# Kernel tuning notes

Measured on AMD Instinct MI355X. Metric: run time of the kernel, lower is better.

The kernel has to match this reference:

```python
import jax, jax.numpy as jnp
import numpy as np


def gru_last(x, lens, Wg, bg, Wc, bc):
    """TF GRUCell scan over time, masked by lens; returns final hidden state.
    x: [N, T, D], lens: [N] int, Wg: [D+H, 2H], Wc: [D+H, H]. Returns [N, H]."""
    N, T, _ = x.shape
    H = bc.shape[0]
    xT = jnp.swapaxes(x, 0, 1)  # [T, N, D]

    def step(h, inp):
        xt, t = inp
        ru = jax.nn.sigmoid(jnp.concatenate([xt, h], axis=-1) @ Wg + bg)
        r, u = jnp.split(ru, 2, axis=-1)
        c = jnp.tanh(jnp.concatenate([xt, r * h], axis=-1) @ Wc + bc)
        hn = u * h + (1.0 - u) * c
        hn = jnp.where((t < lens)[:, None], hn, h)
        return hn, None

    h0 = jnp.zeros((N, H), x.dtype)
    hT, _ = jax.lax.scan(step, h0, (xT, jnp.arange(T)))
    return hT


def reverse_by_len(x, lens):
    """tf.reverse_sequence: reverse first lens[i] steps of each row. x: [N,T,D]."""
    T = x.shape[1]
    i = jnp.arange(T)[None, :]
    idx = jnp.where(i < lens[:, None], lens[:, None] - 1 - i, i)
    return jnp.take_along_axis(x, idx[:, :, None], axis=1)


def setup_inputs() -> dict:
    key = jax.random.key(0)
    ks = jax.random.split(key, 16)
    B, S, W = 64, 32, 64
    V, D, H, O = 50000, 128, 256, 5
    s = 0.05
    inp = {
        'X': jax.random.randint(ks[0], (B, S, W), 0, V, dtype=jnp.int32),
        'L': jnp.maximum(1, jax.random.randint(ks[1], (B, S), 0, W, dtype=jnp.int32)),
        'L2': jnp.maximum(1, jax.random.randint(ks[2], (B,), 0, S, dtype=jnp.int32)),
        'emb': jax.random.normal(ks[3], (V, D), jnp.float32) * s,
        'sWg_f': jax.random.normal(ks[4], (2 * D, 2 * D), jnp.float32) * s,
        'sbg_f': jnp.ones((2 * D,), jnp.float32),
        'sWc_f': jax.random.normal(ks[5], (2 * D, D), jnp.float32) * s,
        'sbc_f': jnp.zeros((D,), jnp.float32),
        'sWg_b': jax.random.normal(ks[6], (2 * D, 2 * D), jnp.float32) * s,
        'sbg_b': jnp.ones((2 * D,), jnp.float32),
        'sWc_b': jax.random.normal(ks[7], (2 * D, D), jnp.float32) * s,
        'sbc_b': jnp.zeros((D,), jnp.float32),
        'dWg_f': jax.random.normal(ks[8], (2 * D + H, 2 * H), jnp.float32) * s,
        'dbg_f': jnp.ones((2 * H,), jnp.float32),
        'dWc_f': jax.random.normal(ks[9], (2 * D + H, H), jnp.float32) * s,
        'dbc_f': jnp.zeros((H,), jnp.float32),
        'dWg_b': jax.random.normal(ks[10], (2 * D + H, 2 * H), jnp.float32) * s,
        'dbg_b': jnp.ones((2 * H,), jnp.float32),
        'dWc_b': jax.random.normal(ks[11], (2 * D + H, H), jnp.float32) * s,
        'dbc_b': jnp.zeros((H,), jnp.float32),
        'W1': jax.random.normal(ks[12], (2 * H, H), jnp.float32) * s,
        'b1': jnp.zeros((H,), jnp.float32),
        'W2': jax.random.normal(ks[13], (H, O), jnp.float32) * s,
        'b2': jnp.zeros((O,), jnp.float32),
    }
    return inp


def reference(X, L, L2, emb,
              sWg_f, sbg_f, sWc_f, sbc_f, sWg_b, sbg_b, sWc_b, sbc_b,
              dWg_f, dbg_f, dWc_f, dbc_f, dWg_b, dbg_b, dWc_b, dbc_b,
              W1, b1, W2, b2):
    B, S, W = X.shape
    D = emb.shape[1]
    # word embeddings: [B, S, W, D] -> flatten sentences to rows
    words = emb[X].reshape(B * S, W, D)
    ls = L.reshape(B * S)
    # sentence-level bi-GRU, gather final valid states
    fw = gru_last(words, ls, sWg_f, sbg_f, sWc_f, sbc_f)
    bw = gru_last(reverse_by_len(words, ls), ls, sWg_b, sbg_b, sWc_b, sbc_b)
    sent = jnp.concatenate([fw, bw], axis=-1).reshape(B, S, 2 * D)
    # document-level bi-GRU over sentence vectors
    fw_d = gru_last(sent, L2, dWg_f, dbg_f, dWc_f, dbc_f)
    bw_d = gru_last(reverse_by_len(sent, L2), L2, dWg_b, dbg_b, dWc_b, dbc_b)
    doc = jnp.concatenate([fw_d, bw_d], axis=-1)  # [B, 2H]
    # MLP head
    hidden = jax.nn.relu(doc @ W1 + b1)
    logits = hidden @ W2 + b2
    return logits
```

## Files before the change

kernel.cpp:

```cpp
#include <hip/hip_runtime.h>
#include <cstdint>
#include <cstddef>


typedef __attribute__((ext_vector_type(8))) short bf16x8;
typedef __attribute__((ext_vector_type(8))) _Float16 f16x8;
typedef __attribute__((ext_vector_type(4))) float f32x4;

__device__ __forceinline__ void split_bf16(float f, short& hi, short& lo) {
  unsigned u = __float_as_uint(f);
  unsigned rb = (u + 0x7FFFu + ((u >> 16) & 1u)) & 0xFFFF0000u;
  hi = (short)(rb >> 16);
  float r = f - __uint_as_float(rb);
  unsigned ur = __float_as_uint(r);
  lo = (short)((ur + 0x7FFFu + ((ur >> 16) & 1u)) >> 16);
}

__device__ __forceinline__ void split_f16(float f, short& hi, short& lo) {
  _Float16 h = (_Float16)f;
  hi = __builtin_bit_cast(short, h);
  _Float16 l = (_Float16)(f - (float)h);
  lo = __builtin_bit_cast(short, l);
}

__device__ __forceinline__ float sigm(float x) { return 1.f / (1.f + __expf(-x)); }
__device__ __forceinline__ float tanh_fast(float x) {
  float e = __expf(2.f * x);
  return 1.f - 2.f / (e + 1.f);
}

__global__ void bt_prep(const float* __restrict__ sWg_f, const float* __restrict__ sWc_f,
                        const float* __restrict__ sWg_b, const float* __restrict__ sWc_b,
                        short* __restrict__ BtHi, short* __restrict__ BtLo) {
  int i = blockIdx.x * 256 + threadIdx.x;
  if (i >= 768 * 128) return;
  int n = i >> 7, k = i & 127;
  float f;
  if (n < 256) f = sWg_f[k * 256 + n];
  else if (n < 384) f = sWc_f[k * 128 + (n - 256)];
  else if (n < 640) f = sWg_b[k * 256 + (n - 384)];
  else f = sWc_b[k * 128 + (n - 640)];
  short hi, lo;
  split_bf16(f, hi, lo);
  BtHi[i] = hi;
  BtLo[i] = lo;
}

__global__ void packdt_prep(const float* __restrict__ dWg_f, const float* __restrict__ dWc_f,
                            const float* __restrict__ dWg_b, const float* __restrict__ dWc_b,
                            short* __restrict__ Hi, short* __restrict__ Lo) {
  int i = blockIdx.x * 256 + threadIdx.x;
  if (i >= 1536 * 256) return;
  int n = i >> 8, k = i & 255;
  float f;
  if (n < 512) f = dWg_f[k * 512 + n];
  else if (n < 768) f = dWc_f[k * 256 + (n - 512)];
  else if (n < 1280) f = dWg_b[k * 512 + (n - 768)];
  else f = dWc_b[k * 256 + (n - 1280)];
  short hi, lo;
  split_bf16(f, hi, lo);
  Hi[i] = hi;
  Lo[i] = lo;
}

__global__ __launch_bounds__(256, 1) void emb_gemm(
    const float* __restrict__ emb, const short* __restrict__ BtHi,
    const short* __restrict__ BtLo, float* __restrict__ C) {
  const int tid = threadIdx.x;
  const int w = tid >> 6, l = tid & 63, li = l & 15, g = l >> 4;
  const int m0 = blockIdx.x * 64;

  bf16x8 ahi[4][4], alo[4][4];
#pragma unroll
  for (int mt = 0; mt < 4; ++mt) {
    int row = m0 + 16 * mt + li;
    if (row > 49999) row = 49999;
    const float* ap = emb + (size_t)row * 128 + 8 * g;
#pragma unroll
    for (int kk = 0; kk < 4; ++kk) {
      float4 v0 = *(const float4*)(ap + 32 * kk);
      float4 v1 = *(const float4*)(ap + 32 * kk + 4);
      float vv[8] = {v0.x, v0.y, v0.z, v0.w, v1.x, v1.y, v1.z, v1.w};
#pragma unroll
      for (int e = 0; e < 8; ++e) {
        short hi, lo;
        split_bf16(vv[e], hi, lo);
        ahi[mt][kk][e] = hi;
        alo[mt][kk][e] = lo;
      }
    }
  }

  f32x4 acc[4][12];
#pragma unroll
  for (int mt = 0; mt < 4; ++mt)
#pragma unroll
    for (int nt = 0; nt < 12; ++nt) acc[mt][nt] = (f32x4){0.f, 0.f, 0.f, 0.f};

#pragma unroll
  for (int nt = 0; nt < 12; ++nt) {
    const int col = 192 * w + 16 * nt + li;
    const short* bh = BtHi + col * 128 + 8 * g;
    const short* bl = BtLo + col * 128 + 8 * g;
    bf16x8 bhi[4], blo[4];
#pragma unroll
    for (int kk = 0; kk < 4; ++kk) {
      bhi[kk] = *(const bf16x8*)(bh + 32 * kk);
      blo[kk] = *(const bf16x8*)(bl + 32 * kk);
    }
#pragma unroll
    for (int kk = 0; kk < 4; ++kk)
#pragma unroll
      for (int mt = 0; mt < 4; ++mt) {
        acc[mt][nt] = __builtin_amdgcn_mfma_f32_16x16x32_bf16(alo[mt][kk], bhi[kk], acc[mt][nt], 0, 0, 0);
        acc[mt][nt] = __builtin_amdgcn_mfma_f32_16x16x32_bf16(ahi[mt][kk], blo[kk], acc[mt][nt], 0, 0, 0);
        acc[mt][nt] = __builtin_amdgcn_mfma_f32_16x16x32_bf16(ahi[mt][kk], bhi[kk], acc[mt][nt], 0, 0, 0);
      }
  }

#pragma unroll
  for (int mt = 0; mt < 4; ++mt)
#pragma unroll
    for (int nt = 0; nt < 12; ++nt) {
      const int col = 192 * w + 16 * nt + li;
#pragma unroll
      for (int r = 0; r < 4; ++r) {
        int row = m0 + 16 * mt + 4 * g + r;
        if (row < 50000) C[(size_t)row * 768 + col] = acc[mt][nt][r];
      }
    }
}

__global__ __launch_bounds__(256, 1) void xproj_gemm(
    const short* __restrict__ AHi, const short* __restrict__ ALo,
    const short* __restrict__ BtHi, const short* __restrict__ BtLo,
    float* __restrict__ C) {
  const int tid = threadIdx.x;
  const int w = tid >> 6, l = tid & 63, li = l & 15, g = l >> 4;
  const int m0 = blockIdx.x * 64;
  const int n0 = blockIdx.y * 512 + 128 * w;

  f32x4 acc[4][8];
#pragma unroll
  for (int mt = 0; mt < 4; ++mt)
#pragma unroll
    for (int nt = 0; nt < 8; ++nt) acc[mt][nt] = (f32x4){0.f, 0.f, 0.f, 0.f};

#pragma unroll
  for (int kk = 0; kk < 8; ++kk) {
    bf16x8 ah[4], al[4];
#pragma unroll
    for (int mt = 0; mt < 4; ++mt) {
      const int row = m0 + 16 * mt + li;
      ah[mt] = *(const bf16x8*)&AHi[(size_t)row * 256 + 32 * kk + 8 * g];
      al[mt] = *(const bf16x8*)&ALo[(size_t)row * 256 + 32 * kk + 8 * g];
    }
#pragma unroll
    for (int nt = 0; nt < 8; ++nt) {
      const int col = n0 + 16 * nt + li;
      bf16x8 bh = *(const bf16x8*)&BtHi[(size_t)col * 256 + 32 * kk + 8 * g];
      bf16x8 bl = *(const bf16x8*)&BtLo[(size_t)col * 256 + 32 * kk + 8 * g];
#pragma unroll
      for (int mt = 0; mt < 4; ++mt) {
        acc[mt][nt] = __builtin_amdgcn_mfma_f32_16x16x32_bf16(al[mt], bh, acc[mt][nt], 0, 0, 0);
        acc[mt][nt] = __builtin_amdgcn_mfma_f32_16x16x32_bf16(ah[mt], bl, acc[mt][nt], 0, 0, 0);
        acc[mt][nt] = __builtin_amdgcn_mfma_f32_16x16x32_bf16(ah[mt], bh, acc[mt][nt], 0, 0, 0);
      }
    }
  }

#pragma unroll
  for (int mt = 0; mt < 4; ++mt)
#pragma unroll
    for (int nt = 0; nt < 8; ++nt) {
      const int col = n0 + 16 * nt + li;
#pragma unroll
      for (int r = 0; r < 4; ++r) {
        int row = m0 + 16 * mt + 4 * g + r;
        C[(size_t)row * 1536 + col] = acc[mt][nt][r];
      }
    }
}

#define SENTS 16

__global__ __launch_bounds__(256, 1) void sent_gru(
    const int* __restrict__ X, const int* __restrict__ L,
    const float* __restrict__ embProj,
    const float* __restrict__ Wg_f, const float* __restrict__ bg_f,
    const float* __restrict__ Wc_f, const float* __restrict__ bc_f,
    const float* __restrict__ Wg_b, const float* __restrict__ bg_b,
    const float* __restrict__ Wc_b, const float* __restrict__ bc_b,
    short* __restrict__ sentHi, short* __restrict__ sentLo) {
  const int dir = blockIdx.y;
  const int g0 = blockIdx.x * SENTS;
  const int tid = threadIdx.x;
  const int w = tid >> 6, l = tid & 63;
  const int li = l & 15, g = l >> 4;
  const float* Wg = dir ? Wg_b : Wg_f;
  const float* Wc = dir ? Wc_b : Wc_f;
  const float* bgp = dir ? bg_b : bg_f;
  const float* bcp = dir ? bc_b : bc_f;

  __shared__ float xbuf[2][SENTS][384];
  __shared__ float h_f[SENTS][132];
  __shared__ float u_f[SENTS][132];
  alignas(16) __shared__ short h_hi[SENTS][136], h_lo[SENTS][136];
  alignas(16) __shared__ short rh_hi[SENTS][136], rh_lo[SENTS][136];
  __shared__ int wid[2][SENTS];
  __shared__ int len_s[SENTS];

  bf16x8 bgh[4][4], bgl[4][4];
  bf16x8 bch[2][4], bcl[2][4];
#pragma unroll
  for (int nt = 0; nt < 4; ++nt)
#pragma unroll
    for (int kk = 0; kk < 4; ++kk) {
      const float* base = Wg + (size_t)(128 + 32 * kk + 8 * g) * 256 + 64 * w + 16 * nt + li;
#pragma unroll
      for (int e = 0; e < 8; ++e) {
        short hi, lo;
        split_bf16(base[(size_t)e * 256], hi, lo);
        bgh[nt][kk][e] = hi; bgl[nt][kk][e] = lo;
      }
    }
#pragma unroll
  for (int ct = 0; ct < 2; ++ct)
#pragma unroll
    for (int kk = 0; kk < 4; ++kk) {
      const float* base = Wc + (size_t)(128 + 32 * kk + 8 * g) * 128 + 32 * w + 16 * ct + li;
#pragma unroll
      for (int e = 0; e < 8; ++e) {
        short hi, lo;
        split_bf16(base[(size_t)e * 128], hi, lo);
        bch[ct][kk][e] = hi; bcl[ct][kk][e] = lo;
      }
    }
  float bgj[4], bcj[2];
#pragma unroll
  for (int nt = 0; nt < 4; ++nt) bgj[nt] = bgp[64 * w + 16 * nt + li];
#pragma unroll
  for (int ct = 0; ct < 2; ++ct) bcj[ct] = bcp[32 * w + 16 * ct + li];

  if (tid < SENTS) {
    int ll = L[g0 + tid];
    len_s[tid] = ll;
    wid[0][tid] = X[(g0 + tid) * 64 + (dir ? (ll - 1) : 0)];
    wid[1][tid] = (1 < ll) ? X[(g0 + tid) * 64 + (dir ? (ll - 2) : 1)] : 0;
  }
  for (int q = tid; q < SENTS * 136; q += 256) {
    ((short*)h_hi)[q] = 0; ((short*)h_lo)[q] = 0;
  }
  for (int q = tid; q < SENTS * 132; q += 256) ((float*)h_f)[q] = 0.f;
  __syncthreads();

  int lens4[4];
#pragma unroll
  for (int r = 0; r < 4; ++r) lens4[r] = len_s[4 * g + r];
  int maxlen = 0;
#pragma unroll
  for (int m = 0; m < SENTS; ++m) maxlen = max(maxlen, len_s[m]);

  auto prefetch_x = [&](int t) {
    int b = t & 1;
#pragma unroll
    for (int c = 0; c < 6; ++c) {
      int q = tid + 256 * c;
      int m = q / 96, s = q - m * 96;
      const float* src = embProj + (size_t)wid[b][m] * 768 + dir * 384 + s * 4;
      float* dst = (float*)&xbuf[b][0][0] + q * 4;
      __builtin_amdgcn_global_load_lds(
          (const __attribute__((address_space(1))) void*)src,
          (__attribute__((address_space(3))) void*)dst, 16, 0, 0);
    }
  };

  prefetch_x(0);
  __syncthreads();

  for (int t = 0; t < maxlen; ++t) {
    const int cur = t & 1;
    prefetch_x(t + 1);
    if (tid < SENTS) {
      int ll = len_s[tid], tt = t + 2;
      wid[tt & 1][tid] = (tt < ll) ? X[(g0 + tid) * 64 + (dir ? (ll - 1 - tt) : tt)] : 0;
    }

    bf16x8 a_hi[4], a_lo[4];
#pragma unroll
    for (int kk = 0; kk < 4; ++kk) {
      a_hi[kk] = *(const bf16x8*)&h_hi[li][32 * kk + 8 * g];
      a_lo[kk] = *(const bf16x8*)&h_lo[li][32 * kk + 8 * g];
    }
    f32x4 accg[4];
#pragma unroll
    for (int nt = 0; nt < 4; ++nt) {
      const int col = 64 * w + 16 * nt + li;
      f32x4 c;
#pragma unroll
      for (int r = 0; r < 4; ++r) c[r] = bgj[nt] + xbuf[cur][4 * g + r][col];
#pragma unroll
      for (int kk = 0; kk < 4; ++kk) {
        c = __builtin_amdgcn_mfma_f32_16x16x32_bf16(a_hi[kk], bgh[nt][kk], c, 0, 0, 0);
        c = __builtin_amdgcn_mfma_f32_16x16x32_bf16(a_hi[kk], bgl[nt][kk], c, 0, 0, 0);
        c = __builtin_amdgcn_mfma_f32_16x16x32_bf16(a_lo[kk], bgh[nt][kk], c, 0, 0, 0);
      }
      accg[nt] = c;
    }
    if (w < 2) {
#pragma unroll
      for (int nt = 0; nt < 4; ++nt) {
        const int col = 64 * w + 16 * nt + li;
#pragma unroll
        for (int r = 0; r < 4; ++r) {
          const int row = 4 * g + r;
          float s = sigm(accg[nt][r]);
          float rh = s * h_f[row][col];
          short hi, lo;
          split_bf16(rh, hi, lo);
          rh_hi[row][col] = hi;
          rh_lo[row][col] = lo;
        }
      }
    } else {
#pragma unroll
      for (int nt = 0; nt < 4; ++nt) {
        const int col = 64 * (w - 2) + 16 * nt + li;
#pragma unroll
        for (int r = 0; r < 4; ++r) {
          u_f[4 * g + r][col] = sigm(accg[nt][r]);
        }
      }
    }
    __syncthreads();

    bf16x8 ra_hi[4], ra_lo[4];
#pragma unroll
    for (int kk = 0; kk < 4; ++kk) {
      ra_hi[kk] = *(const bf16x8*)&rh_hi[li][32 * kk + 8 * g];
      ra_lo[kk] = *(const bf16x8*)&rh_lo[li][32 * kk + 8 * g];
    }
#pragma unroll
    for (int ct = 0; ct < 2; ++ct) {
      const int col = 32 * w + 16 * ct + li;
      f32x4 c;
#pragma unroll
      for (int r = 0; r < 4; ++r) c[r] = bcj[ct] + xbuf[cur][4 * g + r][256 + col];
#pragma unroll
      for (int kk = 0; kk < 4; ++kk) {
        c = __builtin_amdgcn_mfma_f32_16x16x32_bf16(ra_hi[kk], bch[ct][kk], c, 0, 0, 0);
        c = __builtin_amdgcn_mfma_f32_16x16x32_bf16(ra_hi[kk], bcl[ct][kk], c, 0, 0, 0);
        c = __builtin_amdgcn_mfma_f32_16x16x32_bf16(ra_lo[kk], bch[ct][kk], c, 0, 0, 0);
      }
#pragma unroll
      for (int r = 0; r < 4; ++r) {
        const int row = 4 * g + r;
        float cand = tanh_fast(c[r]);
        float u = u_f[row][col];
        float hold = h_f[row][col];
        float hn = u * hold + (1.f - u) * cand;
        hn = (t < lens4[r]) ? hn : hold;
        h_f[row][col] = hn;
        short hi, lo;
        split_bf16(hn, hi, lo);
        h_hi[row][col] = hi;
        h_lo[row][col] = lo;
      }
    }
    __syncthreads();
  }

  for (int q = tid; q < SENTS * 128; q += 256) {
    int m = q >> 7, j = q & 127;
    size_t o = (size_t)(g0 + m) * 256 + dir * 128 + j;
    sentHi[o] = h_hi[m][j];
    sentLo[o] = h_lo[m][j];
  }
}

#define DOCS 16

__global__ __launch_bounds__(512, 1) void doc_gru_mfma(
    const float* __restrict__ xprojD, const int* __restrict__ L2,
    const float* __restrict__ dWg_f, const float* __restrict__ dbg_f,
    const float* __restrict__ dWc_f, const float* __restrict__ dbc_f,
    const float* __restrict__ dWg_b, const float* __restrict__ dbg_b,
    const float* __restrict__ dWc_b, const float* __restrict__ dbc_b,
    float* __restrict__ docv) {
  const int dir = blockIdx.y;
  const int g0 = blockIdx.x * DOCS;
  const int tid = threadIdx.x;
  const int w = tid >> 6, l = tid & 63, li = l & 15, g = l >> 4;
  const float* Wg = dir ? dWg_b : dWg_f;
  const float* Wc = dir ? dWc_b : dWc_f;
  const float* bgp = dir ? dbg_b : dbg_f;
  const float* bcp = dir ? dbc_b : dbc_f;
  const int xoff = dir ? 768 : 0;

  alignas(16) __shared__ short h_hi[DOCS][264], h_lo[DOCS][264];
  alignas(16) __shared__ short rh_hi[DOCS][264], rh_lo[DOCS][264];
  __shared__ float h_f[DOCS][256], u_f[DOCS][256];
  __shared__ int len_s[DOCS];

  f16x8 wg[4][8];
  f16x8 wc[2][8];
  const float* Wg_h = Wg + 256 * 512;
  const float* Wc_h = Wc + 256 * 256;
#pragma unroll
  for (int nt = 0; nt < 4; ++nt)
#pragma unroll
    for (int kk = 0; kk < 8; ++kk) {
      const float* base = Wg_h + (size_t)(32 * kk + 8 * g) * 512 + 64 * w + 16 * nt + li;
#pragma unroll
      for (int e = 0; e < 8; ++e) wg[nt][kk][e] = (_Float16)base[(size_t)e * 512];
      asm volatile("" : "+v"(wg[nt][kk]));
    }
#pragma unroll
  for (int ct = 0; ct < 2; ++ct)
#pragma unroll
    for (int kk = 0; kk < 8; ++kk) {
      const float* base = Wc_h + (size_t)(32 * kk + 8 * g) * 256 + 32 * w + 16 * ct + li;
#pragma unroll
      for (int e = 0; e < 8; ++e) wc[ct][kk][e] = (_Float16)base[(size_t)e * 256];
      asm volatile("" : "+v"(wc[ct][kk]));
    }
  float bgj[4], bcj[2];
#pragma unroll
  for (int nt = 0; nt < 4; ++nt) bgj[nt] = bgp[64 * w + 16 * nt + li];
#pragma unroll
  for (int ct = 0; ct < 2; ++ct) bcj[ct] = bcp[32 * w + 16 * ct + li];

  if (tid < DOCS) len_s[tid] = L2[g0 + tid];
  for (int q = tid; q < DOCS * 264; q += 512) {
    ((short*)h_hi)[q] = 0; ((short*)h_lo)[q] = 0;
  }
  for (int q = tid; q < DOCS * 256; q += 512) {
    ((float*)h_f)[q] = 0.f; ((float*)u_f)[q] = 0.f;
  }
  __syncthreads();

  int lens4[4];
#pragma unroll
  for (int r = 0; r < 4; ++r) lens4[r] = len_s[4 * g + r];
  int maxlen = 0;
#pragma unroll
  for (int m = 0; m < DOCS; ++m) maxlen = max(maxlen, len_s[m]);

  for (int t = 0; t < maxlen; ++t) {
    size_t xbase[4];
#pragma unroll
    for (int r = 0; r < 4; ++r) {
      int ti = dir ? max(lens4[r] - 1 - t, 0) : t;
      xbase[r] = ((size_t)(g0 + 4 * g + r) * 32 + ti) * 1536 + xoff;
    }

    f32x4 acc[4];
#pragma unroll
    for (int nt = 0; nt < 4; ++nt) {
      const int col = 64 * w + 16 * nt + li;
#pragma unroll
      for (int r = 0; r < 4; ++r) acc[nt][r] = bgj[nt] + xprojD[xbase[r] + col];
    }
    f32x4 acc2[2];
#pragma unroll
    for (int ct = 0; ct < 2; ++ct) {
      const int col = 32 * w + 16 * ct + li;
#pragma unroll
      for (int r = 0; r < 4; ++r) acc2[ct][r] = bcj[ct] + xprojD[xbase[r] + 512 + col];
    }

#pragma unroll
    for (int c = 0; c < 8; ++c) {
      f16x8 ah = *(const f16x8*)&h_hi[li][32 * c + 8 * g];
      f16x8 al = *(const f16x8*)&h_lo[li][32 * c + 8 * g];
#pragma unroll
      for (int nt = 0; nt < 4; ++nt) {
        acc[nt] = __builtin_amdgcn_mfma_f32_16x16x32_f16(al, wg[nt][c], acc[nt], 0, 0, 0);
        acc[nt] = __builtin_amdgcn_mfma_f32_16x16x32_f16(ah, wg[nt][c], acc[nt], 0, 0, 0);
      }
    }
    if (w < 4) {
#pragma unroll
      for (int nt = 0; nt < 4; ++nt) {
        const int col = 64 * w + 16 * nt + li;
#pragma unroll
        for (int r = 0; r < 4; ++r) {
          const int m = 4 * g + r;
          float s = sigm(acc[nt][r]);
          float rh = s * h_f[m][col];
          short hi, lo;
          split_f16(rh, hi, lo);
          rh_hi[m][col] = hi;
          rh_lo[m][col] = lo;
        }
      }
    } else {
#pragma unroll
      for (int nt = 0; nt < 4; ++nt) {
        const int col = 64 * (w - 4) + 16 * nt + li;
#pragma unroll
        for (int r = 0; r < 4; ++r) u_f[4 * g + r][col] = sigm(acc[nt][r]);
      }
    }
    __syncthreads();

#pragma unroll
    for (int c = 0; c < 8; ++c) {
      f16x8 rah = *(const f16x8*)&rh_hi[li][32 * c + 8 * g];
      f16x8 ral = *(const f16x8*)&rh_lo[li][32 * c + 8 * g];
#pragma unroll
      for (int ct = 0; ct < 2; ++ct) {
        acc2[ct] = __builtin_amdgcn_mfma_f32_16x16x32_f16(ral, wc[ct][c], acc2[ct], 0, 0, 0);
        acc2[ct] = __builtin_amdgcn_mfma_f32_16x16x32_f16(rah, wc[ct][c], acc2[ct], 0, 0, 0);
      }
    }
#pragma unroll
    for (int ct = 0; ct < 2; ++ct) {
      const int col = 32 * w + 16 * ct + li;
#pragma unroll
      for (int r = 0; r < 4; ++r) {
        const int m = 4 * g + r;
        float cand = tanh_fast(acc2[ct][r]);
        float u = u_f[m][col];
        float hold = h_f[m][col];
        float hn = u * hold + (1.f - u) * cand;
        hn = (t < lens4[r]) ? hn : hold;
        h_f[m][col] = hn;
        short hi, lo;
        split_f16(hn, hi, lo);
        h_hi[m][col] = hi;
        h_lo[m][col] = lo;
      }
    }
    __syncthreads();
  }

  for (int q = tid; q < DOCS * 256; q += 512) {
    int m = q >> 8, j = q & 255;
    docv[(size_t)(g0 + m) * 512 + dir * 256 + j] = h_f[m][j];
  }
}

__global__ __launch_bounds__(256) void mlp_head(
    const float* __restrict__ docv, const float* __restrict__ W1,
    const float* __restrict__ b1, const float* __restrict__ W2,
    const float* __restrict__ b2, float* __restrict__ out) {
  const int b = blockIdx.x, j = threadIdx.x;
  __shared__ float hid[256];
  float acc = b1[j];
#pragma unroll 4
  for (int k = 0; k < 512; ++k) acc += docv[b * 512 + k] * W1[k * 256 + j];
  hid[j] = fmaxf(acc, 0.f);
  __syncthreads();
  if (j < 5) {
    float a = b2[j];
#pragma unroll 4
    for (int k = 0; k < 256; ++k) a += hid[k] * W2[k * 5 + j];
    out[b * 5 + j] = a;
  }
}

extern "C" void kernel_launch(void* const* d_in, const int* in_sizes, int n_in,
                              void* d_out, int out_size, void* d_ws, size_t ws_size,
                              hipStream_t stream) {
  const int* X = (const int*)d_in[0];
  const int* L = (const int*)d_in[1];
  const int* L2 = (const int*)d_in[2];
  const float* emb = (const float*)d_in[3];
  const float* sWg_f = (const float*)d_in[4];
  const float* sbg_f = (const float*)d_in[5];
  const float* sWc_f = (const float*)d_in[6];
  const float* sbc_f = (const float*)d_in[7];
  const float* sWg_b = (const float*)d_in[8];
  const float* sbg_b = (const float*)d_in[9];
  const float* sWc_b = (const float*)d_in[10];
  const float* sbc_b = (const float*)d_in[11];
  const float* dWg_f = (const float*)d_in[12];
  const float* dbg_f = (const float*)d_in[13];
  const float* dWc_f = (const float*)d_in[14];
  const float* dbc_f = (const float*)d_in[15];
  const float* dWg_b = (const float*)d_in[16];
  const float* dbg_b = (const float*)d_in[17];
  const float* dWc_b = (const float*)d_in[18];
  const float* dbc_b = (const float*)d_in[19];
  const float* W1 = (const float*)d_in[20];
  const float* b1 = (const float*)d_in[21];
  const float* W2 = (const float*)d_in[22];
  const float* b2 = (const float*)d_in[23];
  float* out = (float*)d_out;

  float* ws = (float*)d_ws;
  float* embProj = ws;
  float* xprojD = embProj + 38400000;
  float* docv = xprojD + 3145728;
  short* sentHi = (short*)(docv + 32768);
  short* sentLo = sentHi + 524288;
  short* BtHi = sentLo + 524288;
  short* BtLo = BtHi + 98304;
  short* PdTHi = BtLo + 98304;
  short* PdTLo = PdTHi + 393216;

  hipLaunchKernelGGL(bt_prep, dim3(384), dim3(256), 0, stream,
                     sWg_f, sWc_f, sWg_b, sWc_b, BtHi, BtLo);
  hipLaunchKernelGGL(packdt_prep, dim3(1536), dim3(256), 0, stream,
                     dWg_f, dWc_f, dWg_b, dWc_b, PdTHi, PdTLo);

  hipLaunchKernelGGL(emb_gemm, dim3(782), dim3(256), 0, stream,
                     emb, BtHi, BtLo, embProj);

  hipLaunchKernelGGL(sent_gru, dim3(128, 2), dim3(256), 0, stream,
                     X, L, embProj,
                     sWg_f, sbg_f, sWc_f, sbc_f,
                     sWg_b, sbg_b, sWc_b, sbc_b, sentHi, sentLo);

  hipLaunchKernelGGL(xproj_gemm, dim3(32, 3), dim3(256), 0, stream,
                     sentHi, sentLo, PdTHi, PdTLo, xprojD);

  hipLaunchKernelGGL(doc_gru_mfma, dim3(4, 2), dim3(512), 0, stream,
                     xprojD, L2,
                     dWg_f, dbg_f, dWc_f, dbc_f,
                     dWg_b, dbg_b, dWc_b, dbc_b, docv);

  hipLaunchKernelGGL(mlp_head, dim3(64), dim3(256), 0, stream,
                     docv, W1, b1, W2, b2, out);
}
```

Measured before the change: 773.4 us.

## Drop fp16 hi/lo split in doc GRU and prefetch next-step input projections

The doc-level GRU recurrence now feeds the hidden state and r*h into the MFMAs as a single fp16 value, removing the low-part residual. This halves the MFMA count, the LDS traffic and the split arithmetic per timestep. It also prefetches the next timestep's input projections into registers so global loads overlap the current step. The cost is lower precision in the recurrent matmul, roughly fp16 accuracy on h, which could push results past tolerance, plus extra register pressure from the prefetch buffers.

```diff
diff --git a/kernel.cpp b/kernel.cpp
--- a/kernel.cpp
+++ b/kernel.cpp
@@ -14,13 +14,6 @@
   float r = f - __uint_as_float(rb);
   unsigned ur = __float_as_uint(r);
   lo = (short)((ur + 0x7FFFu + ((ur >> 16) & 1u)) >> 16);
-}
-
-__device__ __forceinline__ void split_f16(float f, short& hi, short& lo) {
-  _Float16 h = (_Float16)f;
-  hi = __builtin_bit_cast(short, h);
-  _Float16 l = (_Float16)(f - (float)h);
-  lo = __builtin_bit_cast(short, l);
 }
 
 __device__ __forceinline__ float sigm(float x) { return 1.f / (1.f + __expf(-x)); }
@@ -397,8 +390,8 @@
   const float* bcp = dir ? dbc_b : dbc_f;
   const int xoff = dir ? 768 : 0;
 
-  alignas(16) __shared__ short h_hi[DOCS][264], h_lo[DOCS][264];
-  alignas(16) __shared__ short rh_hi[DOCS][264], rh_lo[DOCS][264];
+  alignas(16) __shared__ short h_hi[DOCS][264];
+  alignas(16) __shared__ short rh_hi[DOCS][264];
   __shared__ float h_f[DOCS][256], u_f[DOCS][256];
   __shared__ int len_s[DOCS];
 
@@ -431,9 +424,7 @@
   for (int ct = 0; ct < 2; ++ct) bcj[ct] = bcp[32 * w + 16 * ct + li];
 
   if (tid < DOCS) len_s[tid] = L2[g0 + tid];
-  for (int q = tid; q < DOCS * 264; q += 512) {
-    ((short*)h_hi)[q] = 0; ((short*)h_lo)[q] = 0;
-  }
+  for (int q = tid; q < DOCS * 264; q += 512) ((short*)h_hi)[q] = 0;
   for (int q = tid; q < DOCS * 256; q += 512) {
     ((float*)h_f)[q] = 0.f; ((float*)u_f)[q] = 0.f;
   }
@@ -446,38 +437,48 @@
 #pragma unroll
   for (int m = 0; m < DOCS; ++m) maxlen = max(maxlen, len_s[m]);
 
+  auto xrow = [&](int r, int t) -> size_t {
+    int ti = dir ? max(lens4[r] - 1 - t, 0) : min(t, 31);
+    return ((size_t)(g0 + 4 * g + r) * 32 + ti) * 1536 + xoff;
+  };
+
+  float xg[16], xc[8], xgn[16], xcn[8];
+#pragma unroll
+  for (int r = 0; r < 4; ++r) {
+    size_t xb = xrow(r, 0);
+#pragma unroll
+    for (int nt = 0; nt < 4; ++nt) xg[nt * 4 + r] = xprojD[xb + 64 * w + 16 * nt + li];
+#pragma unroll
+    for (int ct = 0; ct < 2; ++ct) xc[ct * 4 + r] = xprojD[xb + 512 + 32 * w + 16 * ct + li];
+  }
+
   for (int t = 0; t < maxlen; ++t) {
-    size_t xbase[4];
+    f32x4 acc[4];
+#pragma unroll
+    for (int nt = 0; nt < 4; ++nt)
+#pragma unroll
+      for (int r = 0; r < 4; ++r) acc[nt][r] = bgj[nt] + xg[nt * 4 + r];
+    f32x4 acc2[2];
+#pragma unroll
+    for (int ct = 0; ct < 2; ++ct)
+#pragma unroll
+      for (int r = 0; r < 4; ++r) acc2[ct][r] = bcj[ct] + xc[ct * 4 + r];
+
 #pragma unroll
     for (int r = 0; r < 4; ++r) {
-      int ti = dir ? max(lens4[r] - 1 - t, 0) : t;
-      xbase[r] = ((size_t)(g0 + 4 * g + r) * 32 + ti) * 1536 + xoff;
-    }
-
-    f32x4 acc[4];
-#pragma unroll
-    for (int nt = 0; nt < 4; ++nt) {
-      const int col = 64 * w + 16 * nt + li;
-#pragma unroll
-      for (int r = 0; r < 4; ++r) acc[nt][r] = bgj[nt] + xprojD[xbase[r] + col];
-    }
-    f32x4 acc2[2];
-#pragma unroll
-    for (int ct = 0; ct < 2; ++ct) {
-      const int col = 32 * w + 16 * ct + li;
-#pragma unroll
-      for (int r = 0; r < 4; ++r) acc2[ct][r] = bcj[ct] + xprojD[xbase[r] + 512 + col];
+      size_t xb = xrow(r, t + 1);
+#pragma unroll
+      for (int nt = 0; nt < 4; ++nt) xgn[nt * 4 + r] = xprojD[xb + 64 * w + 16 * nt + li];
+#pragma unroll
+      for (int ct = 0; ct < 2; ++ct) xcn[ct * 4 + r] = xprojD[xb + 512 + 32 * w + 16 * ct + li];
     }
 
 #pragma unroll
     for (int c = 0; c < 8; ++c) {
       f16x8 ah = *(const f16x8*)&h_hi[li][32 * c + 8 * g];
-      f16x8 al = *(const f16x8*)&h_lo[li][32 * c + 8 * g];
-#pragma unroll
-      for (int nt = 0; nt < 4; ++nt) {
-        acc[nt] = __builtin_amdgcn_mfma_f32_16x16x32_f16(al, wg[nt][c], acc[nt], 0, 0, 0);
+#pragma unroll
+      for (int nt = 0; nt < 4; ++nt)
         acc[nt] = __builtin_amdgcn_mfma_f32_16x16x32_f16(ah, wg[nt][c], acc[nt], 0, 0, 0);
-      }
     }
     if (w < 4) {
 #pragma unroll
@@ -488,10 +489,7 @@
           const int m = 4 * g + r;
           float s = sigm(acc[nt][r]);
           float rh = s * h_f[m][col];
-          short hi, lo;
-          split_f16(rh, hi, lo);
-          rh_hi[m][col] = hi;
-          rh_lo[m][col] = lo;
+          rh_hi[m][col] = __builtin_bit_cast(short, (_Float16)rh);
         }
       }
     } else {
@@ -507,12 +505,9 @@
 #pragma unroll
     for (int c = 0; c < 8; ++c) {
       f16x8 rah = *(const f16x8*)&rh_hi[li][32 * c + 8 * g];
-      f16x8 ral = *(const f16x8*)&rh_lo[li][32 * c + 8 * g];
-#pragma unroll
-      for (int ct = 0; ct < 2; ++ct) {
-        acc2[ct] = __builtin_amdgcn_mfma_f32_16x16x32_f16(ral, wc[ct][c], acc2[ct], 0, 0, 0);
+#pragma unroll
+      for (int ct = 0; ct < 2; ++ct)
         acc2[ct] = __builtin_amdgcn_mfma_f32_16x16x32_f16(rah, wc[ct][c], acc2[ct], 0, 0, 0);
-      }
     }
 #pragma unroll
     for (int ct = 0; ct < 2; ++ct) {
@@ -526,13 +521,15 @@
         float hn = u * hold + (1.f - u) * cand;
         hn = (t < lens4[r]) ? hn : hold;
         h_f[m][col] = hn;
-        short hi, lo;
-        split_f16(hn, hi, lo);
-        h_hi[m][col] = hi;
-        h_lo[m][col] = lo;
+        h_hi[m][col] = __builtin_bit_cast(short, (_Float16)hn);
       }
     }
     __syncthreads();
+
+#pragma unroll
+    for (int i = 0; i < 16; ++i) xg[i] = xgn[i];
+#pragma unroll
+    for (int i = 0; i < 8; ++i) xc[i] = xcn[i];
   }
 
   for (int q = tid; q < DOCS * 256; q += 512) {
```

New measurement: 774.9 us. About the same (+0.2%).
